# Optimization experiments

Measured on AMD Instinct MI355X. Metric: run time of the kernel, lower is better.

Reference implementation:

```python
import jax, jax.numpy as jnp
import numpy as np

MARGIN = 0.3

def _cdist(x):
    # pairwise euclidean distances, safe sqrt (zero grad at 0)
    sq = jnp.sum(x * x, axis=1)
    d2 = sq[:, None] + sq[None, :] - 2.0 * (x @ x.T)
    d2 = jnp.maximum(d2, 0.0)
    safe = jnp.where(d2 > 0, d2, 1.0)
    return jnp.where(d2 > 0, jnp.sqrt(safe), 0.0)

def setup_inputs() -> dict:
    key = jax.random.key(0)
    k1, k2 = jax.random.split(key)
    embeddings = jax.random.normal(k1, (4096, 128), dtype=jnp.float32)
    labels = jax.random.randint(k2, (4096,), 0, 256)
    return {"embeddings": embeddings, "labels": labels}

def reference(embeddings, labels):
    B = embeddings.shape[0]
    dist = _cdist(embeddings)                      # [B, B]
    same = labels[:, None] == labels[None, :]      # [B, B]
    eye = jnp.eye(B, dtype=bool)
    pos_mask = same & ~eye
    neg_mask = ~same
    neg_inf = jnp.array(-jnp.inf, dist.dtype)
    pos_inf = jnp.array(jnp.inf, dist.dtype)
    hard_pos = jnp.max(jnp.where(pos_mask, dist, neg_inf), axis=1)  # [B]
    hard_neg = jnp.min(jnp.where(neg_mask, dist, pos_inf), axis=1)  # [B]
    valid = jnp.any(pos_mask, axis=1) & jnp.any(neg_mask, axis=1)
    per_row = jax.nn.relu(hard_pos - hard_neg + MARGIN)
    per_row = jnp.where(valid, per_row, 0.0)
    num_valid = jnp.sum(valid.astype(dist.dtype))
    return jnp.sum(per_row) / jnp.maximum(num_valid, 1.0)
```

## Files before the change

kernel.cpp:

```cpp
#include <hip/hip_runtime.h>
#include <hip/hip_bf16.h>


typedef __attribute__((ext_vector_type(8))) short short8;
typedef __attribute__((ext_vector_type(4))) float f32x4;

#define MARGIN_F 0.3f
#define NEG_BIG -3.4e38f
#define POS_BIG 3.4e38f
#define WAITVM(N) __builtin_amdgcn_s_waitcnt(((N)&15)|((((N)>>4)&3)<<14)|(7<<4)|(15<<8))

__device__ __forceinline__ void gl_lds16(const void* g, void* l) {
    __builtin_amdgcn_global_load_lds(
        (const __attribute__((address_space(1))) void*)g,
        (__attribute__((address_space(3))) void*)l, 16, 0, 0);
}

__device__ inline unsigned short f2bf(float x) {
    union { __hip_bfloat16 h; unsigned short u; } c;
    c.h = __float2bfloat16(x);
    return c.u;
}

__global__ __launch_bounds__(256) void tl_prep(const float* __restrict__ E,
                                               unsigned short* __restrict__ Ebf,
                                               float* __restrict__ sqn,
                                               unsigned* __restrict__ accum) {
    int t = blockIdx.x * 256 + threadIdx.x;
    if (t < 4) accum[t] = 0u;
    int row = t >> 5;
    int kq = (t & 31) * 4;
    float4 v = *(const float4*)&E[(size_t)row * 128 + kq];
    float s = fmaf(v.x, v.x, fmaf(v.y, v.y, fmaf(v.z, v.z, v.w * v.w)));
    ushort4 h4;
    h4.x = f2bf(v.x); h4.y = f2bf(v.y); h4.z = f2bf(v.z); h4.w = f2bf(v.w);
    *(ushort4*)&Ebf[(size_t)row * 128 + kq] = h4;
#pragma unroll
    for (int m = 1; m < 32; m <<= 1) s += __shfl_xor(s, m);
    if ((t & 31) == 0) sqn[row] = s;
}

__global__ __launch_bounds__(256, 2) void tl_phase1(const unsigned short* __restrict__ Ebf,
                                                    const int* __restrict__ labels,
                                                    const float* __restrict__ sqn,
                                                    float* __restrict__ pmp,
                                                    float* __restrict__ pmn) {
    union SM {
        struct { unsigned short A[2][128 * 64]; unsigned short B[2][128 * 64]; } s;
        struct { float mp[128][32]; float mn[128][32]; } f;
    };
    __shared__ __align__(16) SM sm;

    const int tid = threadIdx.x;
    const int l = tid & 63, w = tid >> 6;
    const int wr = w >> 1, wc = w & 1;
    const int q = l >> 4, r16 = l & 15;
    const int i0 = blockIdx.x * 128, j0 = blockIdx.y * 128;

    const unsigned short* gA[4];
    const unsigned short* gB[4];
#pragma unroll
    for (int t2 = 0; t2 < 4; ++t2) {
        int s = w * 256 + t2 * 64 + l;
        int row = s >> 3, ch = (s & 7) ^ (row & 7);
        gA[t2] = Ebf + (size_t)(i0 + row) * 128 + ch * 8;
        gB[t2] = Ebf + (size_t)(j0 + row) * 128 + ch * 8;
    }

    int li[4][4], lj[4];
    float sj[4];
#pragma unroll
    for (int ti = 0; ti < 4; ++ti)
#pragma unroll
        for (int p = 0; p < 4; ++p)
            li[ti][p] = labels[i0 + wr * 64 + ti * 16 + q * 4 + p];
#pragma unroll
    for (int tj = 0; tj < 4; ++tj) {
        int cj = j0 + wc * 64 + tj * 16 + r16;
        lj[tj] = labels[cj];
        sj[tj] = sqn[cj];
    }

#pragma unroll
    for (int t2 = 0; t2 < 4; ++t2) {
        gl_lds16(gA[t2], &sm.s.A[0][w * 2048 + t2 * 512]);
        gl_lds16(gB[t2], &sm.s.B[0][w * 2048 + t2 * 512]);
    }
#pragma unroll
    for (int t2 = 0; t2 < 4; ++t2) {
        gl_lds16(gA[t2] + 64, &sm.s.A[1][w * 2048 + t2 * 512]);
        gl_lds16(gB[t2] + 64, &sm.s.B[1][w * 2048 + t2 * 512]);
    }

    f32x4 acc[4][4];
#pragma unroll
    for (int ti = 0; ti < 4; ++ti)
#pragma unroll
        for (int tj = 0; tj < 4; ++tj) acc[ti][tj] = (f32x4)0.0f;

#pragma unroll
    for (int kc = 0; kc < 2; ++kc) {
        if (kc == 0) WAITVM(8); else WAITVM(0);
        __builtin_amdgcn_s_barrier();
#pragma unroll
        for (int s = 0; s < 2; ++s) {
            short8 af[4], bf[4];
            const int cA = ((s * 4 + q) ^ (r16 & 7)) * 8;
#pragma unroll
            for (int t2 = 0; t2 < 4; ++t2) {
                af[t2] = *(const short8*)&sm.s.A[kc][(wr * 64 + t2 * 16 + r16) * 64 + cA];
                bf[t2] = *(const short8*)&sm.s.B[kc][(wc * 64 + t2 * 16 + r16) * 64 + cA];
            }
#pragma unroll
            for (int ti = 0; ti < 4; ++ti)
#pragma unroll
                for (int tj = 0; tj < 4; ++tj)
                    acc[ti][tj] = __builtin_amdgcn_mfma_f32_16x16x32_bf16(
                        af[ti], bf[tj], acc[ti][tj], 0, 0, 0);
        }
    }

    float mp[4][4], mn[4][4];
#pragma unroll
    for (int ti = 0; ti < 4; ++ti)
#pragma unroll
        for (int p = 0; p < 4; ++p) { mp[ti][p] = NEG_BIG; mn[ti][p] = POS_BIG; }
    const bool diagblk = (blockIdx.x == blockIdx.y);
#pragma unroll
    for (int tj = 0; tj < 4; ++tj) {
#pragma unroll
        for (int ti = 0; ti < 4; ++ti)
#pragma unroll
            for (int p = 0; p < 4; ++p) {
                float val = fmaf(-2.0f, acc[ti][tj][p], sj[tj]);
                bool same = (li[ti][p] == lj[tj]);
                bool self = diagblk &&
                    ((wr * 64 + ti * 16 + q * 4 + p) == (wc * 64 + tj * 16 + r16));
                mp[ti][p] = fmaxf(mp[ti][p], (same && !self) ? val : NEG_BIG);
                mn[ti][p] = fminf(mn[ti][p], same ? POS_BIG : val);
            }
    }

    __syncthreads();
#pragma unroll
    for (int ti = 0; ti < 4; ++ti)
#pragma unroll
        for (int p = 0; p < 4; ++p) {
            int rloc = wr * 64 + ti * 16 + q * 4 + p;
            sm.f.mp[rloc][wc * 16 + r16] = mp[ti][p];
            sm.f.mn[rloc][wc * 16 + r16] = mn[ti][p];
        }
    __syncthreads();
    {
        int row = tid >> 1, hf = tid & 1;
        const float4* P = (const float4*)&sm.f.mp[row][hf * 16];
        const float4* N = (const float4*)&sm.f.mn[row][hf * 16];
        float4 p0 = P[0], p1 = P[1], p2 = P[2], p3 = P[3];
        float4 n0 = N[0], n1 = N[1], n2 = N[2], n3 = N[3];
        float M = fmaxf(fmaxf(fmaxf(p0.x, p0.y), fmaxf(p0.z, p0.w)),
                        fmaxf(fmaxf(p1.x, p1.y), fmaxf(p1.z, p1.w)));
        M = fmaxf(M, fmaxf(fmaxf(fmaxf(p2.x, p2.y), fmaxf(p2.z, p2.w)),
                           fmaxf(fmaxf(p3.x, p3.y), fmaxf(p3.z, p3.w))));
        float m_ = fminf(fminf(fminf(n0.x, n0.y), fminf(n0.z, n0.w)),
                         fminf(fminf(n1.x, n1.y), fminf(n1.z, n1.w)));
        m_ = fminf(m_, fminf(fminf(fminf(n2.x, n2.y), fminf(n2.z, n2.w)),
                             fminf(fminf(n3.x, n3.y), fminf(n3.z, n3.w))));
        M = fmaxf(M, __shfl_xor(M, 1));
        m_ = fminf(m_, __shfl_xor(m_, 1));
        if (hf == 0) {
            pmp[(size_t)blockIdx.y * 4096 + i0 + row] = M;
            pmn[(size_t)blockIdx.y * 4096 + i0 + row] = m_;
        }
    }
}

__global__ __launch_bounds__(256) void tl_phase2(const int* __restrict__ labels,
                                                 const float* __restrict__ pmp,
                                                 const float* __restrict__ pmn,
                                                 const float* __restrict__ sqn,
                                                 float* __restrict__ accum,
                                                 float* __restrict__ out) {
    __shared__ unsigned hist[256];
    __shared__ float sp[4], sv[4];
    int tid = threadIdx.x;
    hist[tid] = 0u;
    __syncthreads();
#pragma unroll
    for (int k = 0; k < 16; ++k) atomicAdd(&hist[labels[k * 256 + tid]], 1u);
    __syncthreads();

    int r = blockIdx.x * 256 + tid;
    float mp = NEG_BIG, mn = POS_BIG;
#pragma unroll
    for (int k = 0; k < 32; ++k) {
        mp = fmaxf(mp, pmp[(size_t)k * 4096 + r]);
        mn = fminf(mn, pmn[(size_t)k * 4096 + r]);
    }
    float si = sqn[r];
    unsigned cnt = hist[labels[r]];
    bool valid = (cnt >= 2u) && (cnt < 4096u);
    float hp = sqrtf(fmaxf(si + mp, 0.0f));
    float hn = sqrtf(fmaxf(si + mn, 0.0f));
    float pr = fmaxf(hp - hn + MARGIN_F, 0.0f);
    float s = valid ? pr : 0.0f;
    float n = valid ? 1.0f : 0.0f;
#pragma unroll
    for (int m = 1; m < 64; m <<= 1) {
        s += __shfl_xor(s, m);
        n += __shfl_xor(n, m);
    }
    if ((tid & 63) == 0) { sp[tid >> 6] = s; sv[tid >> 6] = n; }
    __syncthreads();
    if (tid == 0) {
        float ts = sp[0] + sp[1] + sp[2] + sp[3];
        float tn = sv[0] + sv[1] + sv[2] + sv[3];
        atomicAdd(&accum[0], ts);
        atomicAdd(&accum[1], tn);
        __threadfence();
        unsigned tk = atomicAdd((unsigned*)&accum[2], 1u);
        if (tk == 15u) {
            float a = atomicAdd(&accum[0], 0.0f);
            float b = atomicAdd(&accum[1], 0.0f);
            out[0] = a / fmaxf(b, 1.0f);
        }
    }
}

extern "C" void kernel_launch(void* const* d_in, const int* in_sizes, int n_in,
                              void* d_out, int out_size, void* d_ws, size_t ws_size,
                              hipStream_t stream) {
    const float* E = (const float*)d_in[0];
    const int* labels = (const int*)d_in[1];
    float* out = (float*)d_out;

    char* base = (char*)d_ws;
    unsigned short* Ebf = (unsigned short*)base;
    float* pmp = (float*)(base + (1u << 20));
    float* pmn = (float*)(base + (1u << 20) + (512u << 10));
    float* sqn = (float*)(base + (2u << 20));
    float* accum = (float*)(base + (2u << 20) + (16u << 10));

    tl_prep<<<512, 256, 0, stream>>>(E, Ebf, sqn, (unsigned*)accum);
    tl_phase1<<<dim3(32, 32), 256, 0, stream>>>(Ebf, labels, sqn, pmp, pmn);
    tl_phase2<<<16, 256, 0, stream>>>(labels, pmp, pmn, sqn, accum, out);
}
```

Before: 73.18 us.

## Exploit distance symmetry: compute only upper-triangular tiles with row and column reductions

Launches only the 528 upper-triangular 128x128 tiles instead of all 1024. Each tile now produces row-wise and column-wise masked max/min partials, and the column partials are written into the transposed tile's slot. This roughly halves the MFMA and load work. In exchange the epilogue does more per tile: extra FMAs, selects, shared-memory traffic, and a triangular index decode per block.

```diff
diff --git a/kernel.cpp b/kernel.cpp
--- a/kernel.cpp
+++ b/kernel.cpp
@@ -47,7 +47,8 @@
                                                     float* __restrict__ pmn) {
     union SM {
         struct { unsigned short A[2][128 * 64]; unsigned short B[2][128 * 64]; } s;
-        struct { float mp[128][32]; float mn[128][32]; } f;
+        struct { float mp[128][32]; float mn[128][32];
+                 float mpc[128][8]; float mnc[128][8]; } f;
     };
     __shared__ __align__(16) SM sm;
 
@@ -55,7 +56,14 @@
     const int l = tid & 63, w = tid >> 6;
     const int wr = w >> 1, wc = w & 1;
     const int q = l >> 4, r16 = l & 15;
-    const int i0 = blockIdx.x * 128, j0 = blockIdx.y * 128;
+
+    int t = (int)blockIdx.x;
+    int bx = (int)((65.0f - sqrtf((float)(4225 - 8 * t))) * 0.5f);
+    while (bx * (65 - bx) / 2 > t) --bx;
+    while ((bx + 1) * (64 - bx) / 2 <= t) ++bx;
+    const int by = bx + (t - bx * (65 - bx) / 2);
+    const int i0 = bx * 128, j0 = by * 128;
+    const bool diagblk = (bx == by);
 
     const unsigned short* gA[4];
     const unsigned short* gB[4];
@@ -68,12 +76,15 @@
     }
 
     int li[4][4], lj[4];
-    float sj[4];
-#pragma unroll
-    for (int ti = 0; ti < 4; ++ti)
-#pragma unroll
-        for (int p = 0; p < 4; ++p)
-            li[ti][p] = labels[i0 + wr * 64 + ti * 16 + q * 4 + p];
+    float si[4][4], sj[4];
+#pragma unroll
+    for (int ti = 0; ti < 4; ++ti)
+#pragma unroll
+        for (int p = 0; p < 4; ++p) {
+            int ci = i0 + wr * 64 + ti * 16 + q * 4 + p;
+            li[ti][p] = labels[ci];
+            si[ti][p] = sqn[ci];
+        }
 #pragma unroll
     for (int tj = 0; tj < 4; ++tj) {
         int cj = j0 + wc * 64 + tj * 16 + r16;
@@ -120,25 +131,31 @@
         }
     }
 
-    float mp[4][4], mn[4][4];
+    float mp[4][4], mn[4][4], mpc[4], mnc[4];
 #pragma unroll
     for (int ti = 0; ti < 4; ++ti)
 #pragma unroll
         for (int p = 0; p < 4; ++p) { mp[ti][p] = NEG_BIG; mn[ti][p] = POS_BIG; }
-    const bool diagblk = (blockIdx.x == blockIdx.y);
 #pragma unroll
     for (int tj = 0; tj < 4; ++tj) {
+        float cp = NEG_BIG, cn = POS_BIG;
 #pragma unroll
         for (int ti = 0; ti < 4; ++ti)
 #pragma unroll
             for (int p = 0; p < 4; ++p) {
-                float val = fmaf(-2.0f, acc[ti][tj][p], sj[tj]);
+                float g = acc[ti][tj][p];
+                float vr = fmaf(-2.0f, g, sj[tj]);
+                float vc = fmaf(-2.0f, g, si[ti][p]);
                 bool same = (li[ti][p] == lj[tj]);
                 bool self = diagblk &&
                     ((wr * 64 + ti * 16 + q * 4 + p) == (wc * 64 + tj * 16 + r16));
-                mp[ti][p] = fmaxf(mp[ti][p], (same && !self) ? val : NEG_BIG);
-                mn[ti][p] = fminf(mn[ti][p], same ? POS_BIG : val);
+                mp[ti][p] = fmaxf(mp[ti][p], (same && !self) ? vr : NEG_BIG);
+                mn[ti][p] = fminf(mn[ti][p], same ? POS_BIG : vr);
+                cp = fmaxf(cp, (same && !self) ? vc : NEG_BIG);
+                cn = fminf(cn, same ? POS_BIG : vc);
             }
+        mpc[tj] = cp;
+        mnc[tj] = cn;
     }
 
     __syncthreads();
@@ -150,6 +167,12 @@
             sm.f.mp[rloc][wc * 16 + r16] = mp[ti][p];
             sm.f.mn[rloc][wc * 16 + r16] = mn[ti][p];
         }
+#pragma unroll
+    for (int tj = 0; tj < 4; ++tj) {
+        int cloc = wc * 64 + tj * 16 + r16;
+        sm.f.mpc[cloc][wr * 4 + q] = mpc[tj];
+        sm.f.mnc[cloc][wr * 4 + q] = mnc[tj];
+    }
     __syncthreads();
     {
         int row = tid >> 1, hf = tid & 1;
@@ -168,9 +191,21 @@
         M = fmaxf(M, __shfl_xor(M, 1));
         m_ = fminf(m_, __shfl_xor(m_, 1));
         if (hf == 0) {
-            pmp[(size_t)blockIdx.y * 4096 + i0 + row] = M;
-            pmn[(size_t)blockIdx.y * 4096 + i0 + row] = m_;
-        }
+            pmp[(size_t)by * 4096 + i0 + row] = M;
+            pmn[(size_t)by * 4096 + i0 + row] = m_;
+        }
+    }
+    if (!diagblk && tid < 128) {
+        const float4* P = (const float4*)&sm.f.mpc[tid][0];
+        const float4* N = (const float4*)&sm.f.mnc[tid][0];
+        float4 p0 = P[0], p1 = P[1];
+        float4 n0 = N[0], n1 = N[1];
+        float M = fmaxf(fmaxf(fmaxf(p0.x, p0.y), fmaxf(p0.z, p0.w)),
+                        fmaxf(fmaxf(p1.x, p1.y), fmaxf(p1.z, p1.w)));
+        float m_ = fminf(fminf(fminf(n0.x, n0.y), fminf(n0.z, n0.w)),
+                         fminf(fminf(n1.x, n1.y), fminf(n1.z, n1.w)));
+        pmp[(size_t)bx * 4096 + j0 + tid] = M;
+        pmn[(size_t)bx * 4096 + j0 + tid] = m_;
     }
 }
 
@@ -241,6 +276,6 @@
     float* accum = (float*)(base + (2u << 20) + (16u << 10));
 
     tl_prep<<<512, 256, 0, stream>>>(E, Ebf, sqn, (unsigned*)accum);
-    tl_phase1<<<dim3(32, 32), 256, 0, stream>>>(Ebf, labels, sqn, pmp, pmn);
+    tl_phase1<<<528, 256, 0, stream>>>(Ebf, labels, sqn, pmp, pmn);
     tl_phase2<<<16, 256, 0, stream>>>(labels, pmp, pmn, sqn, accum, out);
 }
```

Result: no change. 72.20 us (-1.3%).
